# Optimization experiments

Hardware: AMD Instinct MI355X
Metric: run time of the kernel (lower is better)

Reference implementation:

```python
import jax, jax.numpy as jnp
import numpy as np

B, T, LA, L = 4, 32, 32, 512
D, H, C = 2048, 16, 128
KV_DIM = 2048
K = T * LA  # total kv tokens per batch element
EPS = 1e-5


def _ln(x):
    m = jnp.mean(x, axis=-1, keepdims=True)
    v = jnp.var(x, axis=-1, keepdims=True)
    return (x - m) * jax.lax.rsqrt(v + EPS)


def setup_inputs() -> dict:
    key = jax.random.key(0)
    ks = jax.random.split(key, 10)
    s = 1.0 / np.sqrt(D)
    sk = 1.0 / np.sqrt(KV_DIM)
    return {
        "x": jax.random.normal(ks[0], (B, T, LA, KV_DIM), jnp.float32),
        "latents": jax.random.normal(ks[1], (B, L, D), jnp.float32),
        "t_emb": jax.random.normal(ks[2], (B, 3, D), jnp.float32) * 0.02,
        "q_lens": jnp.full((B,), L, dtype=jnp.int32),
        "k_lens": jax.random.randint(ks[3], (B,), K // 2, K + 1).astype(jnp.int32),
        "ln_kv_w": jnp.ones((KV_DIM,), jnp.float32),
        "ln_kv_b": jnp.zeros((KV_DIM,), jnp.float32),
        "ssg": jax.random.normal(ks[4], (1, 3, D), jnp.float32) * s,  # shift_scale_gate param (adaLN=True)
        "Wq": jax.random.normal(ks[5], (D, D), jnp.float32) * s,
        "bq": jnp.zeros((D,), jnp.float32),
        "Wkv": jax.random.normal(ks[6], (KV_DIM, 2 * D), jnp.float32) * sk,
        "bkv": jnp.zeros((2 * D,), jnp.float32),
        "Wo": jax.random.normal(ks[7], (D, D), jnp.float32) * s,
        "bo": jnp.zeros((D,), jnp.float32),
    }


def reference(x, latents, t_emb, q_lens, k_lens, ln_kv_w, ln_kv_b, ssg,
              Wq, bq, Wkv, bkv, Wo, bo):
    # norm_kv (affine LayerNorm over kv_dim)
    xk = _ln(x) * ln_kv_w + ln_kv_b  # (B,T,LA,KV_DIM)
    # AdaLN modulate: shift/scale/gate from t_emb + learned shift_scale_gate
    mod = t_emb + ssg  # (B,3,D)
    shift, scale, gate = mod[:, 0:1], mod[:, 1:2], mod[:, 2:3]  # (B,1,D)
    norm_q = _ln(latents)  # norm_q has no affine when adaLN=True
    lat = norm_q * (1.0 + scale) + shift
    # projections
    q = (lat @ Wq + bq).reshape(B, L, H, C)
    kv = (xk.reshape(B, K, KV_DIM) @ Wkv + bkv)  # (B,K,2D)
    k, v = kv[..., :D], kv[..., D:]
    k = k.reshape(B, K, H, C)
    v = v.reshape(B, K, H, C)
    # varlen attention == per-batch masked attention (keys beyond k_lens masked)
    scores = jnp.einsum("blhc,bkhc->bhlk", q, k) / np.sqrt(C)
    kmask = jnp.arange(K)[None, :] < k_lens[:, None]  # (B,K)
    scores = jnp.where(kmask[:, None, None, :], scores, jnp.finfo(scores.dtype).min)
    attn = jax.nn.softmax(scores, axis=-1)
    out = jnp.einsum("bhlk,bkhc->blhc", attn, v).reshape(B, L, D)
    # queries beyond q_lens are invalid -> zero them (varlen packing semantics)
    qmask = (jnp.arange(L)[None, :] < q_lens[:, None])[..., None]  # (B,L,1)
    out = out * qmask
    return (out @ Wo + bo) * gate
```

## Files before the change

### kernel.cpp

```cpp
#include <hip/hip_runtime.h>

typedef unsigned short u16;
typedef short bf16x8 __attribute__((ext_vector_type(8)));
typedef float f32x4 __attribute__((ext_vector_type(4)));

#define MFMA_BF16(a, b, c) __builtin_amdgcn_mfma_f32_16x16x32_bf16((a), (b), (c), 0, 0, 0)
#define ATT_SCALE 0.08838834764831845f

__device__ __forceinline__ u16 f2bf(float f) {
  union { float f; unsigned int u; } cv;
  cv.f = f;
  unsigned int u = cv.u + 0x7fffu + ((cv.u >> 16) & 1u);
  return (u16)(u >> 16);
}

__global__ __launch_bounds__(256) void prep_kernel(
    const float* __restrict__ x, const float* __restrict__ ln_w,
    const float* __restrict__ ln_b, const float* __restrict__ latents,
    const float* __restrict__ t_emb, const float* __restrict__ ssg,
    const float* __restrict__ Wq, const float* __restrict__ Wo,
    const float* __restrict__ Wkv,
    u16* __restrict__ xk_out, u16* __restrict__ lat_out,
    u16* __restrict__ WqT, u16* __restrict__ WoT, u16* __restrict__ WkvT)
{
  __shared__ float shmem[32 * 33];
  const int blk = blockIdx.x;
  const int tid = threadIdx.x;
  if (blk < 6144) {
    const bool is_x = blk < 4096;
    const int row = is_x ? blk : blk - 4096;
    const float* src = is_x ? (x + (size_t)row * 2048) : (latents + (size_t)row * 2048);
    const float4* xr = (const float4*)src;
    float4 v0 = xr[tid];
    float4 v1 = xr[tid + 256];
    float sum = v0.x + v0.y + v0.z + v0.w + v1.x + v1.y + v1.z + v1.w;
    float sq  = v0.x*v0.x + v0.y*v0.y + v0.z*v0.z + v0.w*v0.w
              + v1.x*v1.x + v1.y*v1.y + v1.z*v1.z + v1.w*v1.w;
    #pragma unroll
    for (int off = 32; off > 0; off >>= 1) {
      sum += __shfl_xor(sum, off);
      sq  += __shfl_xor(sq, off);
    }
    if ((tid & 63) == 0) { shmem[tid >> 6] = sum; shmem[(tid >> 6) + 4] = sq; }
    __syncthreads();
    sum = shmem[0] + shmem[1] + shmem[2] + shmem[3];
    sq  = shmem[4] + shmem[5] + shmem[6] + shmem[7];
    const float mean = sum * (1.0f / 2048.0f);
    const float var  = sq * (1.0f / 2048.0f) - mean * mean;
    const float rstd = rsqrtf(var + 1e-5f);
    if (is_x) {
      const float4* w4 = (const float4*)ln_w;
      const float4* b4 = (const float4*)ln_b;
      ushort4* orow = (ushort4*)(xk_out + (size_t)row * 2048);
      #pragma unroll
      for (int j = 0; j < 2; ++j) {
        const int idx = tid + j * 256;
        const float4 v = j ? v1 : v0;
        const float4 ww = w4[idx];
        const float4 bb = b4[idx];
        ushort4 o;
        o.x = f2bf((v.x - mean) * rstd * ww.x + bb.x);
        o.y = f2bf((v.y - mean) * rstd * ww.y + bb.y);
        o.z = f2bf((v.z - mean) * rstd * ww.z + bb.z);
        o.w = f2bf((v.w - mean) * rstd * ww.w + bb.w);
        orow[idx] = o;
      }
    } else {
      const int bidx = row >> 9;
      const float4* te = (const float4*)(t_emb + (size_t)bidx * 3 * 2048);
      const float4* sg = (const float4*)ssg;
      ushort4* orow = (ushort4*)(lat_out + (size_t)row * 2048);
      #pragma unroll
      for (int j = 0; j < 2; ++j) {
        const int idx = tid + j * 256;
        const float4 v = j ? v1 : v0;
        const float4 t0 = te[idx];
        const float4 t1 = te[512 + idx];
        const float4 s0 = sg[idx];
        const float4 s1 = sg[512 + idx];
        ushort4 o;
        o.x = f2bf(((v.x - mean) * rstd) * (1.0f + t1.x + s1.x) + (t0.x + s0.x));
        o.y = f2bf(((v.y - mean) * rstd) * (1.0f + t1.y + s1.y) + (t0.y + s0.y));
        o.z = f2bf(((v.z - mean) * rstd) * (1.0f + t1.z + s1.z) + (t0.z + s0.z));
        o.w = f2bf(((v.w - mean) * rstd) * (1.0f + t1.w + s1.w) + (t0.w + s0.w));
        orow[idx] = o;
      }
    }
  } else {
    int t = blk - 6144;
    const float* in;
    u16* outp;
    int C, cx, ry;
    if (t < 4096)      { in = Wq;  outp = WqT;  C = 2048; cx = t & 63;  ry = t >> 6; }
    else if (t < 8192) { t -= 4096; in = Wo;  outp = WoT;  C = 2048; cx = t & 63;  ry = t >> 6; }
    else               { t -= 8192; in = Wkv; outp = WkvT; C = 4096; cx = t & 127; ry = t >> 7; }
    float (*tile)[33] = (float(*)[33])shmem;
    const int R = 2048;
    const int c0 = cx * 32;
    const int r0 = ry * 32;
    const int tx = tid & 31;
    const int ty = tid >> 5;
    #pragma unroll
    for (int i = 0; i < 4; ++i)
      tile[ty + i * 8][tx] = in[(size_t)(r0 + ty + i * 8) * C + c0 + tx];
    __syncthreads();
    #pragma unroll
    for (int i = 0; i < 4; ++i)
      outp[(size_t)(c0 + ty + i * 8) * R + r0 + tx] = f2bf(tile[tx][ty + i * 8]);
  }
}

template<int BM, int TMPL>
__global__ __launch_bounds__(256) void gemm_kernel(
    const u16* __restrict__ A0, const u16* __restrict__ BT0,
    const u16* __restrict__ A1, const u16* __restrict__ BT1,
    const float* __restrict__ bias0, const float* __restrict__ bias1,
    u16* __restrict__ out_q, u16* __restrict__ out_k, u16* __restrict__ out_vT,
    float* __restrict__ out_f,
    const float* __restrict__ t_emb, const float* __restrict__ ssg)
{
  constexpr int TI = BM / 32;
  constexpr int Kd = 2048;
  __shared__ u16 As[2][BM][40];
  __shared__ u16 Bs[2][128][40];
  const int tid  = threadIdx.x;
  const int lane = tid & 63;
  const int wv   = tid >> 6;
  const int wm   = wv & 1, wn = wv >> 1;
  const int quad = lane >> 4, lq = lane & 15;

  int mode, m0, n0;
  const u16 *A, *BT;
  const float* bias;
  if (TMPL == 3) {
    int t = blockIdx.x;
    if (t < 256) { mode = 0; A = A0; BT = BT0; bias = bias0;
                   m0 = (t >> 4) * 128; n0 = (t & 15) * 128; }
    else { t -= 256; mode = 1; A = A1; BT = BT1; bias = bias1;
           m0 = (t >> 5) * 128; n0 = (t & 31) * 128; }
  } else {
    mode = 2; A = A0; BT = BT0; bias = bias0;
    m0 = blockIdx.y * BM; n0 = blockIdx.x * 128;
  }

  f32x4 acc[TI][4];
  #pragma unroll
  for (int i = 0; i < TI; ++i)
    #pragma unroll
    for (int j = 0; j < 4; ++j)
      acc[i][j] = (f32x4){0.f, 0.f, 0.f, 0.f};

  const int rB  = tid >> 1;
  const int hfB = (tid & 1) * 16;
  const u16* gB = BT + (size_t)(n0 + rB) * Kd + hfB;
  const int rA  = (BM == 128) ? (tid >> 1) : (tid >> 2);
  const int hA  = (BM == 128) ? 0 : ((tid >> 1) & 1);
  const int hfA = (tid & 1) * 16;
  const u16* gA = A + (size_t)(m0 + rA) * Kd + hA * 32 + hfA;

  uint4 a00, a01, a10, a11, b00, b01, b10, b11;
  a00 = *(const uint4*)(gA);
  a01 = *(const uint4*)(gA + 8);
  if (BM == 128) {
    a10 = *(const uint4*)(gA + 32);
    a11 = *(const uint4*)(gA + 40);
  }
  b00 = *(const uint4*)(gB);
  b01 = *(const uint4*)(gB + 8);
  b10 = *(const uint4*)(gB + 32);
  b11 = *(const uint4*)(gB + 40);

  for (int k0 = 0; k0 < Kd; k0 += 64) {
    __syncthreads();
    *(uint4*)&As[hA][rA][hfA]     = a00;
    *(uint4*)&As[hA][rA][hfA + 8] = a01;
    if (BM == 128) {
      *(uint4*)&As[1][rA][hfA]     = a10;
      *(uint4*)&As[1][rA][hfA + 8] = a11;
    }
    *(uint4*)&Bs[0][rB][hfB]     = b00;
    *(uint4*)&Bs[0][rB][hfB + 8] = b01;
    *(uint4*)&Bs[1][rB][hfB]     = b10;
    *(uint4*)&Bs[1][rB][hfB + 8] = b11;
    __syncthreads();

    const int kn = (k0 + 64 < Kd) ? k0 + 64 : 0;
    a00 = *(const uint4*)(gA + kn);
    a01 = *(const uint4*)(gA + kn + 8);
    if (BM == 128) {
      a10 = *(const uint4*)(gA + kn + 32);
      a11 = *(const uint4*)(gA + kn + 40);
    }
    b00 = *(const uint4*)(gB + kn);
    b01 = *(const uint4*)(gB + kn + 8);
    b10 = *(const uint4*)(gB + kn + 32);
    b11 = *(const uint4*)(gB + kn + 40);

    #pragma unroll
    for (int kk = 0; kk < 2; ++kk) {
      bf16x8 av[TI], bv[4];
      #pragma unroll
      for (int i = 0; i < TI; ++i)
        av[i] = *(const bf16x8*)&As[kk][wm * (BM / 2) + i * 16 + lq][quad * 8];
      #pragma unroll
      for (int j = 0; j < 4; ++j)
        bv[j] = *(const bf16x8*)&Bs[kk][wn * 64 + j * 16 + lq][quad * 8];
      #pragma unroll
      for (int i = 0; i < TI; ++i)
        #pragma unroll
        for (int j = 0; j < 4; ++j)
          acc[i][j] = MFMA_BF16(av[i], bv[j], acc[i][j]);
    }
  }

  #pragma unroll
  for (int i = 0; i < TI; ++i) {
    const int mlb = m0 + wm * (BM / 2) + i * 16 + quad * 4;
    #pragma unroll
    for (int j = 0; j < 4; ++j) {
      const int n = n0 + wn * 64 + j * 16 + lq;
      const float bs = bias[n];
      if (mode == 0) {
        const int h = n >> 7, c = n & 127;
        #pragma unroll
        for (int rr = 0; rr < 4; ++rr) {
          const int m = mlb + rr;
          const int bb = m >> 9, l = m & 511;
          out_q[((size_t)(bb * 16 + h) * 512 + l) * 128 + c] =
              f2bf((acc[i][j][rr] + bs) * ATT_SCALE);
        }
      } else if (mode == 1) {
        if (n < 2048) {
          const int h = n >> 7, c = n & 127;
          #pragma unroll
          for (int rr = 0; rr < 4; ++rr) {
            const int m = mlb + rr;
            const int bb = m >> 10, kk = m & 1023;
            out_k[((size_t)(bb * 16 + h) * 1024 + kk) * 128 + c] = f2bf(acc[i][j][rr] + bs);
          }
        } else {
          const int n2 = n - 2048;
          const int h = n2 >> 7, c = n2 & 127;
          #pragma unroll
          for (int rr = 0; rr < 4; ++rr) {
            const int m = mlb + rr;
            const int bb = m >> 10, kk = m & 1023;
            out_vT[((size_t)(bb * 16 + h) * 128 + c) * 1024 + kk] = f2bf(acc[i][j][rr] + bs);
          }
        }
      } else {
        #pragma unroll
        for (int rr = 0; rr < 4; ++rr) {
          const int m = mlb + rr;
          const int bb = m >> 9;
          const float g = t_emb[((size_t)bb * 3 + 2) * 2048 + n] + ssg[2 * 2048 + n];
          out_f[(size_t)m * 2048 + n] = (acc[i][j][rr] + bs) * g;
        }
      }
    }
  }
}

__global__ __launch_bounds__(256) void attn_kernel(
    const u16* __restrict__ qb, const u16* __restrict__ kb,
    const u16* __restrict__ vT, const int* __restrict__ k_lens,
    const int* __restrict__ q_lens, u16* __restrict__ ao)
{
  __shared__ u16 Ks[64][132];
  __shared__ u16 Vs[128][68];
  __shared__ u16 Ps[64][68];
  const int tid  = threadIdx.x;
  const int w    = tid >> 6;
  const int lane = tid & 63;
  const int quad = lane >> 4, lq = lane & 15;
  const int bh = blockIdx.y;
  const int b  = bh >> 4;
  const int l0 = blockIdx.x * 64;
  const int kl = k_lens[b];
  const int ql = q_lens[b];

  bf16x8 qf[4];
  {
    const u16* qp = qb + ((size_t)bh * 512 + l0 + w * 16 + lq) * 128 + quad * 8;
    #pragma unroll
    for (int ks = 0; ks < 4; ++ks)
      qf[ks] = *(const bf16x8*)(qp + ks * 32);
  }

  const int krow = tid >> 4;
  const int kcol = tid & 15;
  const u16* kg = kb + ((size_t)bh * 1024 + krow) * 128 + kcol * 8;
  const int vrow = tid >> 3;
  const int vcol = tid & 7;
  const u16* vg = vT + (size_t)bh * 128 * 1024 + (size_t)vrow * 1024 + vcol * 8;

  f32x4 o[8];
  #pragma unroll
  for (int j = 0; j < 8; ++j) o[j] = (f32x4){0.f, 0.f, 0.f, 0.f};
  float mrun[4], lrun[4];
  #pragma unroll
  for (int rr = 0; rr < 4; ++rr) { mrun[rr] = -__builtin_inff(); lrun[rr] = 0.f; }

  const int nkt = (kl + 63) >> 6;
  for (int kt = 0; kt < nkt; ++kt) {
    const int k0 = kt * 64;
    uint4 kd[4], vd[4];
    #pragma unroll
    for (int p = 0; p < 4; ++p)
      kd[p] = *(const uint4*)(kg + (size_t)(k0 + p * 16) * 128);
    #pragma unroll
    for (int p = 0; p < 4; ++p)
      vd[p] = *(const uint4*)(vg + (size_t)p * 32 * 1024 + k0);
    __syncthreads();
    #pragma unroll
    for (int p = 0; p < 4; ++p)
      *(uint4*)&Ks[krow + p * 16][kcol * 8] = kd[p];
    #pragma unroll
    for (int p = 0; p < 4; ++p)
      *(uint4*)&Vs[vrow + p * 32][vcol * 8] = vd[p];
    __syncthreads();

    f32x4 s[4];
    #pragma unroll
    for (int ct = 0; ct < 4; ++ct) {
      s[ct] = (f32x4){0.f, 0.f, 0.f, 0.f};
      #pragma unroll
      for (int ks = 0; ks < 4; ++ks) {
        const bf16x8 kf = *(const bf16x8*)&Ks[ct * 16 + lq][ks * 32 + quad * 8];
        s[ct] = MFMA_BF16(qf[ks], kf, s[ct]);
      }
    }
    #pragma unroll
    for (int ct = 0; ct < 4; ++ct) {
      const bool valid = (k0 + ct * 16 + lq) < kl;
      #pragma unroll
      for (int rr = 0; rr < 4; ++rr)
        s[ct][rr] = valid ? s[ct][rr] : -__builtin_inff();
    }
    float mnew[4], alpha[4], rs[4];
    #pragma unroll
    for (int rr = 0; rr < 4; ++rr) {
      float tm = fmaxf(fmaxf(s[0][rr], s[1][rr]), fmaxf(s[2][rr], s[3][rr]));
      tm = fmaxf(tm, __shfl_xor(tm, 1));
      tm = fmaxf(tm, __shfl_xor(tm, 2));
      tm = fmaxf(tm, __shfl_xor(tm, 4));
      tm = fmaxf(tm, __shfl_xor(tm, 8));
      const float mn = fmaxf(mrun[rr], tm);
      alpha[rr] = __expf(mrun[rr] - mn);
      mrun[rr] = mn;
      mnew[rr] = mn;
      rs[rr] = 0.f;
    }
    #pragma unroll
    for (int ct = 0; ct < 4; ++ct)
      #pragma unroll
      for (int rr = 0; rr < 4; ++rr) {
        const float p = __expf(s[ct][rr] - mnew[rr]);
        s[ct][rr] = p;
        rs[rr] += p;
      }
    #pragma unroll
    for (int rr = 0; rr < 4; ++rr) {
      float t = rs[rr];
      t += __shfl_xor(t, 1);
      t += __shfl_xor(t, 2);
      t += __shfl_xor(t, 4);
      t += __shfl_xor(t, 8);
      lrun[rr] = lrun[rr] * alpha[rr] + t;
    }
    #pragma unroll
    for (int j = 0; j < 8; ++j)
      #pragma unroll
      for (int rr = 0; rr < 4; ++rr)
        o[j][rr] *= alpha[rr];

    #pragma unroll
    for (int ct = 0; ct < 4; ++ct)
      #pragma unroll
      for (int rr = 0; rr < 4; ++rr)
        Ps[w * 16 + quad * 4 + rr][ct * 16 + lq] = f2bf(s[ct][rr]);

    bf16x8 pf[2];
    pf[0] = *(const bf16x8*)&Ps[w * 16 + lq][quad * 8];
    pf[1] = *(const bf16x8*)&Ps[w * 16 + lq][32 + quad * 8];

    #pragma unroll
    for (int j = 0; j < 8; ++j) {
      #pragma unroll
      for (int kk = 0; kk < 2; ++kk) {
        const bf16x8 vf = *(const bf16x8*)&Vs[j * 16 + lq][kk * 32 + quad * 8];
        o[j] = MFMA_BF16(pf[kk], vf, o[j]);
      }
    }
  }

  const int h = bh & 15;
  #pragma unroll
  for (int rr = 0; rr < 4; ++rr) {
    const int row = l0 + w * 16 + quad * 4 + rr;
    const float inv = (row < ql) ? (1.0f / lrun[rr]) : 0.0f;
    u16* op = ao + ((size_t)b * 512 + row) * 2048 + h * 128 + lq;
    #pragma unroll
    for (int j = 0; j < 8; ++j)
      op[j * 16] = f2bf(o[j][rr] * inv);
  }
}

extern "C" void kernel_launch(void* const* d_in, const int* in_sizes, int n_in,
                              void* d_out, int out_size, void* d_ws, size_t ws_size,
                              hipStream_t stream) {
  (void)in_sizes; (void)n_in; (void)out_size; (void)ws_size;
  const float* x       = (const float*)d_in[0];
  const float* latents = (const float*)d_in[1];
  const float* t_emb   = (const float*)d_in[2];
  const int*   q_lens  = (const int*)d_in[3];
  const int*   k_lens  = (const int*)d_in[4];
  const float* ln_w    = (const float*)d_in[5];
  const float* ln_b    = (const float*)d_in[6];
  const float* ssg     = (const float*)d_in[7];
  const float* Wq      = (const float*)d_in[8];
  const float* bq      = (const float*)d_in[9];
  const float* Wkv     = (const float*)d_in[10];
  const float* bkv     = (const float*)d_in[11];
  const float* Wo      = (const float*)d_in[12];
  const float* bo      = (const float*)d_in[13];
  float* out = (float*)d_out;

  u16* ws = (u16*)d_ws;
  const size_t MEG = (size_t)1 << 20;
  u16* WqT  = ws;
  u16* WoT  = ws + 4  * MEG;
  u16* WkvT = ws + 8  * MEG;
  u16* xk   = ws + 16 * MEG;
  u16* lat  = ws + 24 * MEG;
  u16* qb   = ws + 28 * MEG;
  u16* kbuf = ws + 32 * MEG;
  u16* vTb  = ws + 40 * MEG;
  u16* aob  = ws + 48 * MEG;

  prep_kernel<<<dim3(22528), dim3(256), 0, stream>>>(
      x, ln_w, ln_b, latents, t_emb, ssg, Wq, Wo, Wkv,
      xk, lat, WqT, WoT, WkvT);

  gemm_kernel<128, 3><<<dim3(1280), dim3(256), 0, stream>>>(
      lat, WqT, xk, WkvT, bq, bkv, qb, kbuf, vTb, nullptr, nullptr, nullptr);

  attn_kernel<<<dim3(8, 64), dim3(256), 0, stream>>>(qb, kbuf, vTb, k_lens, q_lens, aob);

  gemm_kernel<64, 2><<<dim3(16, 32), dim3(256), 0, stream>>>(
      aob, WoT, nullptr, nullptr, bo, nullptr, nullptr, nullptr, nullptr, out, t_emb, ssg);
}
```

Before: 433.8 us.

## Split Q and KV GEMMs and skip KV row tiles beyond k_lens

Replaces the combined Q+KV GEMM launch with two separate launches: the Q projection now uses a 64-row tile, and the KV projection zeroes the K loop for row tiles whose token index is at or past the batch's k_lens. Skipping the KV tiles for masked keys avoids projection work that attention never uses. It also removes the register double-buffered prefetch of the next K slice, so global load latency is no longer hidden behind the MFMA work. It adds one extra kernel launch.

Result: faster. 416.7 us (-3.9%).

```diff
diff --git a/kernel.cpp b/kernel.cpp
--- a/kernel.cpp
+++ b/kernel.cpp
@@ -110,17 +110,17 @@
   }
 }
 
-template<int BM, int TMPL>
-__global__ __launch_bounds__(256) void gemm_kernel(
-    const u16* __restrict__ A0, const u16* __restrict__ BT0,
-    const u16* __restrict__ A1, const u16* __restrict__ BT1,
-    const float* __restrict__ bias0, const float* __restrict__ bias1,
+template<int BM>
+__global__ __launch_bounds__(256) void gemm_bf16_kernel(
+    const u16* __restrict__ A, const u16* __restrict__ BT,
+    int Kd, int mode,
+    const float* __restrict__ bias,
     u16* __restrict__ out_q, u16* __restrict__ out_k, u16* __restrict__ out_vT,
     float* __restrict__ out_f,
-    const float* __restrict__ t_emb, const float* __restrict__ ssg)
+    const float* __restrict__ t_emb, const float* __restrict__ ssg,
+    const int* __restrict__ k_lens)
 {
   constexpr int TI = BM / 32;
-  constexpr int Kd = 2048;
   __shared__ u16 As[2][BM][40];
   __shared__ u16 Bs[2][128][40];
   const int tid  = threadIdx.x;
@@ -128,20 +128,7 @@
   const int wv   = tid >> 6;
   const int wm   = wv & 1, wn = wv >> 1;
   const int quad = lane >> 4, lq = lane & 15;
-
-  int mode, m0, n0;
-  const u16 *A, *BT;
-  const float* bias;
-  if (TMPL == 3) {
-    int t = blockIdx.x;
-    if (t < 256) { mode = 0; A = A0; BT = BT0; bias = bias0;
-                   m0 = (t >> 4) * 128; n0 = (t & 15) * 128; }
-    else { t -= 256; mode = 1; A = A1; BT = BT1; bias = bias1;
-           m0 = (t >> 5) * 128; n0 = (t & 31) * 128; }
-  } else {
-    mode = 2; A = A0; BT = BT0; bias = bias0;
-    m0 = blockIdx.y * BM; n0 = blockIdx.x * 128;
-  }
+  const int m0 = blockIdx.y * BM, n0 = blockIdx.x * 128;
 
   f32x4 acc[TI][4];
   #pragma unroll
@@ -149,6 +136,9 @@
     #pragma unroll
     for (int j = 0; j < 4; ++j)
       acc[i][j] = (f32x4){0.f, 0.f, 0.f, 0.f};
+
+  int kiters = Kd;
+  if (mode == 1 && (m0 & 1023) >= k_lens[m0 >> 10]) kiters = 0;
 
   const int rB  = tid >> 1;
   const int hfB = (tid & 1) * 16;
@@ -158,19 +148,18 @@
   const int hfA = (tid & 1) * 16;
   const u16* gA = A + (size_t)(m0 + rA) * Kd + hA * 32 + hfA;
 
-  uint4 a00, a01, a10, a11, b00, b01, b10, b11;
-  a00 = *(const uint4*)(gA);
-  a01 = *(const uint4*)(gA + 8);
-  if (BM == 128) {
-    a10 = *(const uint4*)(gA + 32);
-    a11 = *(const uint4*)(gA + 40);
-  }
-  b00 = *(const uint4*)(gB);
-  b01 = *(const uint4*)(gB + 8);
-  b10 = *(const uint4*)(gB + 32);
-  b11 = *(const uint4*)(gB + 40);
-
-  for (int k0 = 0; k0 < Kd; k0 += 64) {
+  for (int k0 = 0; k0 < kiters; k0 += 64) {
+    uint4 a00, a01, a10, a11;
+    a00 = *(const uint4*)(gA + k0);
+    a01 = *(const uint4*)(gA + k0 + 8);
+    if (BM == 128) {
+      a10 = *(const uint4*)(gA + k0 + 32);
+      a11 = *(const uint4*)(gA + k0 + 40);
+    }
+    const uint4 b00 = *(const uint4*)(gB + k0);
+    const uint4 b01 = *(const uint4*)(gB + k0 + 8);
+    const uint4 b10 = *(const uint4*)(gB + k0 + 32);
+    const uint4 b11 = *(const uint4*)(gB + k0 + 40);
     __syncthreads();
     *(uint4*)&As[hA][rA][hfA]     = a00;
     *(uint4*)&As[hA][rA][hfA + 8] = a01;
@@ -183,19 +172,6 @@
     *(uint4*)&Bs[1][rB][hfB]     = b10;
     *(uint4*)&Bs[1][rB][hfB + 8] = b11;
     __syncthreads();
-
-    const int kn = (k0 + 64 < Kd) ? k0 + 64 : 0;
-    a00 = *(const uint4*)(gA + kn);
-    a01 = *(const uint4*)(gA + kn + 8);
-    if (BM == 128) {
-      a10 = *(const uint4*)(gA + kn + 32);
-      a11 = *(const uint4*)(gA + kn + 40);
-    }
-    b00 = *(const uint4*)(gB + kn);
-    b01 = *(const uint4*)(gB + kn + 8);
-    b10 = *(const uint4*)(gB + kn + 32);
-    b11 = *(const uint4*)(gB + kn + 40);
-
     #pragma unroll
     for (int kk = 0; kk < 2; ++kk) {
       bf16x8 av[TI], bv[4];
@@ -442,11 +418,13 @@
       x, ln_w, ln_b, latents, t_emb, ssg, Wq, Wo, Wkv,
       xk, lat, WqT, WoT, WkvT);
 
-  gemm_kernel<128, 3><<<dim3(1280), dim3(256), 0, stream>>>(
-      lat, WqT, xk, WkvT, bq, bkv, qb, kbuf, vTb, nullptr, nullptr, nullptr);
+  gemm_bf16_kernel<64><<<dim3(16, 32), dim3(256), 0, stream>>>(
+      lat, WqT, 2048, 0, bq, qb, nullptr, nullptr, nullptr, nullptr, nullptr, k_lens);
+  gemm_bf16_kernel<128><<<dim3(32, 32), dim3(256), 0, stream>>>(
+      xk, WkvT, 2048, 1, bkv, nullptr, kbuf, vTb, nullptr, nullptr, nullptr, k_lens);
 
   attn_kernel<<<dim3(8, 64), dim3(256), 0, stream>>>(qb, kbuf, vTb, k_lens, q_lens, aob);
 
-  gemm_kernel<64, 2><<<dim3(16, 32), dim3(256), 0, stream>>>(
-      aob, WoT, nullptr, nullptr, bo, nullptr, nullptr, nullptr, nullptr, out, t_emb, ssg);
+  gemm_bf16_kernel<64><<<dim3(16, 32), dim3(256), 0, stream>>>(
+      aob, WoT, 2048, 2, bo, nullptr, nullptr, nullptr, out, t_emb, ssg, k_lens);
 }
```
